# Kernel tuning notes

Hardware: AMD Instinct MI355X
Metric: run time of the kernel (lower is better)

Reference implementation:

```python
import jax, jax.numpy as jnp
import numpy as np

B, C, H, NH = 4, 512, 768, 12        # docs, seq len, hidden, attn heads
NE, MM = 20, 23                      # entities/doc, max mentions/entity
NP_ = NE * (NE - 1)                  # 380 head-tail pairs per doc
QS, POS, EMB, BLK, NB = 128, 128, 768, 64, 12
NCLS = 97
NEG = -10000.0

def _lin(k, i, o):
    return jax.random.normal(k, (i, o), jnp.float32) / np.sqrt(i)

def setup_inputs():
    key = jax.random.key(0)
    ks = jax.random.split(key, 24)
    seq = jax.random.normal(ks[0], (B, C, H), jnp.float32)
    att = jax.random.uniform(ks[1], (B, NH, C, C), jnp.float32)
    midx = jax.random.randint(ks[2], (B, NE, MM), 0, C)
    cnt = jax.random.randint(ks[3], (B, NE), 1, MM + 1)
    mmask = (jnp.arange(MM)[None, None, :] < cnt[:, :, None]).astype(jnp.float32)
    hh, tt = jnp.meshgrid(jnp.arange(NE), jnp.arange(NE), indexing='ij')
    off = ~jnp.eye(NE, dtype=bool)
    hts = jnp.stack([hh[off], tt[off]], -1)
    hts = jnp.broadcast_to(hts[None], (B, NP_, 2))
    vis = (jax.random.uniform(ks[4], (B, NP_, NP_)) > 0.3).astype(jnp.float32)
    inp = dict(sequence_output=seq, attention=att, mention_idx=midx,
               mention_mask=mmask, hts=hts, visible_mask=vis)
    wspec = [('Wcq', H, QS), ('Weq', H, QS), ('Whe', 2 * H, EMB), ('Wte', 2 * H, EMB),
             ('Wbl', EMB * BLK, EMB), ('Wpp', EMB + 2 * POS, EMB),
             ('Wgq', EMB, EMB), ('Wgk', EMB, EMB), ('Wgv', EMB, EMB),
             ('Wp1', 3 * EMB, EMB), ('Wp2', EMB, NCLS)]
    for j, (nm, i, o) in enumerate(wspec):
        inp[nm] = _lin(ks[5 + j], i, o)
        inp['b' + nm[1:]] = jnp.zeros((o,), jnp.float32)
    for nm in ('bgq', 'bgk', 'bgv'):
        inp.pop(nm)
    inp['pos_emb'] = jax.random.normal(ks[20], (42, POS), jnp.float32) * 0.02
    return inp

def reference(sequence_output, attention, mention_idx, mention_mask, hts, visible_mask,
              Wcq, bcq, Weq, beq, Whe, bhe, Wte, bte, Wbl, bbl, Wpp, bpp,
              Wgq, Wgk, Wgv, Wp1, bp1, Wp2, bp2, pos_emb):
    b3 = jnp.arange(B)[:, None, None]
    # per-entity mention gather (padded mentions zeroed, as in the torch loop)
    ent_emb = sequence_output[b3, mention_idx] * mention_mask[..., None]        # [B,NE,MM,H]
    att_t = jnp.transpose(attention, (0, 2, 1, 3))                              # [B,C,NH,C]
    ent_att = att_t[b3, mention_idx] * mention_mask[..., None, None]            # [B,NE,MM,NH,C]
    cnt = mention_mask.sum(-1)[..., None, None]
    ent_att = ent_att.sum(2) / cnt                                              # mean over valid mentions [B,NE,NH,C]

    bi = jnp.arange(B)[:, None]
    hi, ti = hts[..., 0], hts[..., 1]
    hs_m, ts_m = ent_emb[bi, hi], ent_emb[bi, ti]                               # [B,P,MM,H]
    hmask, tmask = mention_mask[bi, hi], mention_mask[bi, ti]                   # [B,P,MM]
    ht_att = (ent_att[bi, hi] * ent_att[bi, ti]).mean(2)                        # mean over heads [B,P,C]
    ht_att = ht_att / (ht_att.sum(-1, keepdims=True) + 1e-5)
    rs = jnp.einsum('bld,bpl->bpd', sequence_output, ht_att)                    # context [B,P,H]

    htq = rs @ Wcq + bcq                                                        # [B,P,QS]
    scale = 1.0 / np.sqrt(EMB)                                                  # original divides by sqrt(emb_size)
    G1 = jnp.einsum('bpq,bpmq->bpm', htq, hs_m @ Weq + beq) * scale
    G2 = jnp.einsum('bpq,bpmq->bpm', htq, ts_m @ Weq + beq) * scale
    G1 = jnp.where(hmask > 0, G1, NEG)
    G2 = jnp.where(tmask > 0, G2, NEG)
    hs = jnp.einsum('bpm,bpmh->bph', jax.nn.softmax(G1, -1), hs_m)
    ts = jnp.einsum('bpm,bpmh->bph', jax.nn.softmax(G2, -1), ts_m)

    hs = jnp.tanh(jnp.concatenate([hs, rs], -1) @ Whe + bhe)                    # [B,P,EMB]
    ts = jnp.tanh(jnp.concatenate([ts, rs], -1) @ Wte + bte)
    bh = hs.reshape(B, NP_, NB, BLK)
    bt = ts.reshape(B, NP_, NB, BLK)
    pair = (bh[..., :, None] * bt[..., None, :]).reshape(B, NP_, EMB * BLK)     # grouped bilinear feature
    pair = pair @ Wbl + bbl                                                     # [B,P,EMB]
    hs_core, ts_core = pos_emb[hi], pos_emb[ti]                                 # [B,P,POS]
    pair = jnp.tanh(jnp.concatenate([hs_core, pair, ts_core], -1) @ Wpp + bpp)

    # pair graph: one masked self-attention layer over pairs with residual
    q, k, v = pair @ Wgq, pair @ Wgk, pair @ Wgv
    sc = jnp.einsum('bpd,bqd->bpq', q, k) / np.sqrt(EMB)
    sc = jnp.where(visible_mask > 0, sc, NEG)
    pair = pair + jnp.einsum('bpq,bqd->bpd', jax.nn.softmax(sc, -1), v)

    feat = jnp.concatenate([hs, ts, pair], -1)                                  # [B,P,3*EMB]
    logits = jnp.tanh(feat @ Wp1 + bp1) @ Wp2 + bp2                             # dropout is identity at eval
    return logits.reshape(B * NP_, NCLS)
```

## Files before the change

kernel.cpp:

```cpp
#include <hip/hip_runtime.h>
#include <hip/hip_bf16.h>

#define Bn   4
#define Cn   512
#define Hn   768
#define NHn  12
#define NEn  20
#define MMn  23
#define Pn   380
#define Mr   1520
#define QSn  128
#define NEGV (-10000.0f)
#define SCL  0.036084391824351615f

typedef unsigned int uint32;
typedef __attribute__((ext_vector_type(8))) short short8;
typedef __attribute__((ext_vector_type(4))) float float4v;
typedef __attribute__((ext_vector_type(2))) _Float16 half2v;
typedef __attribute__((ext_vector_type(2))) __fp16 fp16x2;
typedef __attribute__((ext_vector_type(8))) _Float16 half8;

__device__ __forceinline__ unsigned short f2h(float f){
    return __builtin_bit_cast(unsigned short, (_Float16)f);
}
__device__ __forceinline__ uint32 pkrtz(float a, float b){
    fp16x2 h = __builtin_amdgcn_cvt_pkrtz(a, b);
    return __builtin_bit_cast(uint32, h);
}

static const size_t o_HS = 0;
static const size_t o_TS = 1167360;
static const size_t o_PB = 2334720;
static const size_t Xo   = 3502080;
static const size_t oEA = Xo;
static const size_t oEE = Xo+491520;
static const size_t oEK = Xo+1904640;
static const size_t oHA = Xo+2140160;
static const size_t oHQ = Xo+2918400;
static const size_t oSH = Xo+3112960;
static const size_t oST = Xo+4280320;
static const size_t oRS = Xo+5447680;
static const size_t oSEQT = Xo+6615040;
static const size_t oWCQ = Xo;
static const size_t oWEQ = Xo+49152;
static const size_t oWHE = Xo;
static const size_t oWTE = Xo+589824;
static const size_t oWBL = Xo;
static const size_t oFP = Xo;
static const size_t oPT = Xo+1556480;
static const size_t oQ  = Xo+2723840;
static const size_t oKT = Xo+3891200;
static const size_t oV  = Xo+5058560;
static const size_t oP2 = Xo+6225920;
static const size_t oT1 = Xo+7393280;
static const size_t oWPP = Xo+8560640;
static const size_t oWGQ = Xo+8953856;
static const size_t oWGK = Xo+9248768;
static const size_t oWGV = Xo+9543680;
static const size_t oWP1 = Xo+9838592;
static const size_t oWP2 = Xo+10723328;


__global__ __launch_bounds__(256) void k_ent_att(const float* __restrict__ att,
    const int* __restrict__ midx, const float* __restrict__ mmask, float* __restrict__ ea)
{
    int x = blockIdx.x;
    int nh = x % NHn; int e = (x / NHn) % NEn; int b = x / (NHn * NEn);
    __shared__ int   sidx[MMn];
    __shared__ float smsk[MMn];
    int t = threadIdx.x;
    if (t < MMn) { sidx[t] = midx[(b*NEn+e)*MMn + t]; smsk[t] = mmask[(b*NEn+e)*MMn + t]; }
    __syncthreads();
    float cnt = 0.f;
    for (int m = 0; m < MMn; m++) cnt += smsk[m];
    for (int c = t; c < Cn; c += 256) {
        float acc = 0.f;
        for (int m = 0; m < MMn; m++)
            acc += smsk[m] * att[((size_t)(b*NHn+nh)*Cn + sidx[m])*Cn + c];
        ea[(size_t)x*Cn + c] = acc / cnt;
    }
}

__global__ __launch_bounds__(256) void k_ent_emb(const float* __restrict__ seq,
    const int* __restrict__ midx, const float* __restrict__ mmask, float* __restrict__ ee)
{
    int x = blockIdx.x;
    int b = x / (NEn*MMn);
    int idx = midx[x]; float msk = mmask[x];
    int t = threadIdx.x;
    for (int h = t; h < Hn; h += 256)
        ee[(size_t)x*Hn + h] = msk * seq[((size_t)b*Cn + idx)*Hn + h];
}

__global__ __launch_bounds__(256) void k_htatt(const float* __restrict__ ea,
    const int* __restrict__ hts, float* __restrict__ hta)
{
    int row = blockIdx.x; int b = row / Pn;
    int he = hts[row*2], te = hts[row*2+1];
    __shared__ float sc[Cn];
    __shared__ float red[256];
    int t = threadIdx.x;
    const float* eah = ea + (size_t)(b*NEn+he)*NHn*Cn;
    const float* eat = ea + (size_t)(b*NEn+te)*NHn*Cn;
    for (int c = t; c < Cn; c += 256) {
        float a = 0.f;
        for (int nh = 0; nh < NHn; nh++) a += eah[nh*Cn+c]*eat[nh*Cn+c];
        sc[c] = a * (1.0f/NHn);
    }
    __syncthreads();
    float ps = sc[t] + sc[t+256];
    red[t] = ps; __syncthreads();
    for (int s = 128; s > 0; s >>= 1) { if (t < s) red[t] += red[t+s]; __syncthreads(); }
    float inv = 1.0f/(red[0] + 1e-5f);
    for (int c = t; c < Cn; c += 256) hta[(size_t)row*Cn + c] = sc[c]*inv;
}

__global__ __launch_bounds__(256) void k_select(const float* __restrict__ htq,
    const float* __restrict__ ekey, const float* __restrict__ ee,
    const float* __restrict__ mmask, const int* __restrict__ hts,
    float* __restrict__ selh, float* __restrict__ selt)
{
    int row = blockIdx.x; int side = blockIdx.y;
    int b = row / Pn;
    int e = hts[row*2 + side];
    __shared__ float qv[QSn];
    __shared__ float gsc[MMn];
    __shared__ float ew[MMn];
    int t = threadIdx.x;
    if (t < QSn) qv[t] = htq[(size_t)row*QSn + t];
    __syncthreads();
    if (t < MMn) {
        const float* kr = ekey + ((size_t)(b*NEn+e)*MMn + t)*QSn;
        float g = 0.f;
        for (int qq = 0; qq < QSn; qq++) g += qv[qq]*kr[qq];
        g *= SCL;
        float msk = mmask[(b*NEn+e)*MMn + t];
        gsc[t] = (msk > 0.f) ? g : NEGV;
    }
    __syncthreads();
    float mx = -1e30f;
    for (int m = 0; m < MMn; m++) mx = fmaxf(mx, gsc[m]);
    if (t < MMn) ew[t] = expf(gsc[t] - mx);
    __syncthreads();
    float s = 0.f;
    for (int m = 0; m < MMn; m++) s += ew[m];
    float invs = 1.0f/s;
    float* dst = side ? selt : selh;
    const float* eb = ee + (size_t)(b*NEn+e)*MMn*Hn;
    for (int h = t; h < Hn; h += 256) {
        float o = 0.f;
        for (int m = 0; m < MMn; m++) o += ew[m]*eb[(size_t)m*Hn + h];
        dst[(size_t)row*Hn + h] = o*invs;
    }
}

struct WD { const float* src; unsigned short* dst; int K; int N; int Npad; int t0; };
struct WT8 { WD d[8]; int nd; };

__global__ __launch_bounds__(256) void k_wtr(WT8 tab)
{
    int b = blockIdx.x;
    int i = 0;
    while (i+1 < tab.nd && b >= tab.d[i+1].t0) i++;
    WD d = tab.d[i];
    int tile = b - d.t0;
    int ktiles = d.K >> 6;
    int kt = tile % ktiles, nt = tile / ktiles;
    int k0 = kt*64, n0 = nt*64;
    __shared__ __align__(16) unsigned short tl[64][72];
    int t = threadIdx.x;
    int nl = t & 63, rq = t >> 6;
    #pragma unroll
    for (int r = 0; r < 16; r++) {
        int kl = r*4 + rq;
        float v = (n0+nl < d.N) ? d.src[(size_t)(k0+kl)*d.N + n0 + nl] : 0.f;
        tl[nl][kl] = f2h(v);
    }
    __syncthreads();
    int nn2 = t >> 2, kk0 = (t & 3) * 16;
    uint4 a = *(const uint4*)&tl[nn2][kk0];
    uint4 bq = *(const uint4*)&tl[nn2][kk0+8];
    uint4* dst = (uint4*)&d.dst[(size_t)(n0+nn2)*d.K + k0 + kk0];
    dst[0] = a; dst[1] = bq;
}

template<int MODE, int TM>
__global__ __launch_bounds__(256,4) void k_gmfma(
    const float* __restrict__ A0, const float* __restrict__ A1, const float* __restrict__ A2,
    int KA, int KB, int KC,
    const unsigned short* __restrict__ Wt,
    const float* __restrict__ bias, float* __restrict__ out,
    float* __restrict__ out2, float* __restrict__ out3,
    int Mtot, int N, int kchunk,
    long aStride, long wStride, long oStride)
{
    __shared__ __align__(16) unsigned short sa[64][72];
    __shared__ __align__(16) unsigned short sw[64][72];
    int t = threadIdx.x;
    int K = KA + KB + KC;
    int row0 = blockIdx.x * 64;
    int n0 = blockIdx.y * 64;
    int bz = blockIdx.z;
    const float* Ab = A0; const unsigned short* W = Wt; float* O = out;
    if (MODE & 32) { Ab += (size_t)bz*aStride; W += (size_t)bz*wStride; O += (size_t)bz*oStride; }
    int k0 = 0, k1 = K;
    if (MODE & 1) { k0 = bz*kchunk; k1 = k0 + kchunk; }
    int lane = t & 63, w = t >> 6, ln = lane & 15, q = lane >> 4;
    int sr = t >> 2;
    int sk = (t & 3) * 16;
    int rA = row0 + sr; if (rA > Mtot-1) rA = Mtot-1;

    float4v acc[4];
    #pragma unroll
    for (int mt = 0; mt < 4; mt++) acc[mt] = (float4v)0.f;

    for (int kk = k0; kk < k1; kk += 64) {
        const float* src; int kloc, Kl, seg;
        if (kk < KA)            { src = Ab; kloc = kk;          Kl = KA; seg = 0; }
        else if (kk < KA + KB)  { src = A1; kloc = kk - KA;     Kl = KB; seg = 1; }
        else                    { src = A2; kloc = kk - KA - KB; Kl = KC; seg = 2; }
        const float* ap = &src[(size_t)rA*Kl + kloc + sk];
        float4 v0 = ((const float4*)ap)[0];
        float4 v1 = ((const float4*)ap)[1];
        float4 v2 = ((const float4*)ap)[2];
        float4 v3 = ((const float4*)ap)[3];
        if (TM && ((TM >> seg) & 1)) {
            v0.x = tanhf(v0.x); v0.y = tanhf(v0.y); v0.z = tanhf(v0.z); v0.w = tanhf(v0.w);
            v1.x = tanhf(v1.x); v1.y = tanhf(v1.y); v1.z = tanhf(v1.z); v1.w = tanhf(v1.w);
            v2.x = tanhf(v2.x); v2.y = tanhf(v2.y); v2.z = tanhf(v2.z); v2.w = tanhf(v2.w);
            v3.x = tanhf(v3.x); v3.y = tanhf(v3.y); v3.z = tanhf(v3.z); v3.w = tanhf(v3.w);
        }
        const uint4* gw = (const uint4*)&W[(size_t)(n0+sr)*K + kk + sk];
        uint4 w0 = gw[0], w1 = gw[1];
        uint4 pa, pb;
        pa.x = pkrtz(v0.x, v0.y); pa.y = pkrtz(v0.z, v0.w);
        pa.z = pkrtz(v1.x, v1.y); pa.w = pkrtz(v1.z, v1.w);
        pb.x = pkrtz(v2.x, v2.y); pb.y = pkrtz(v2.z, v2.w);
        pb.z = pkrtz(v3.x, v3.y); pb.w = pkrtz(v3.z, v3.w);
        *(uint4*)&sa[sr][sk]   = pa;
        *(uint4*)&sa[sr][sk+8] = pb;
        *(uint4*)&sw[sr][sk]   = w0;
        *(uint4*)&sw[sr][sk+8] = w1;
        __syncthreads();
        half8 b0 = *(const half8*)&sw[w*16+ln][q*8];
        half8 b1 = *(const half8*)&sw[w*16+ln][32 + q*8];
        #pragma unroll
        for (int mt = 0; mt < 4; mt++) {
            half8 a0 = *(const half8*)&sa[mt*16+ln][q*8];
            half8 a1 = *(const half8*)&sa[mt*16+ln][32 + q*8];
            acc[mt] = __builtin_amdgcn_mfma_f32_16x16x32_f16(a0, b0, acc[mt], 0, 0, 0);
            acc[mt] = __builtin_amdgcn_mfma_f32_16x16x32_f16(a1, b1, acc[mt], 0, 0, 0);
        }
        __syncthreads();
    }
    int nn = n0 + w*16 + ln;
    if (MODE & 16) {
        int sg = nn / Hn; int nl = nn - sg*Hn;
        #pragma unroll
        for (int mt = 0; mt < 4; mt++) {
            #pragma unroll
            for (int r = 0; r < 4; r++) {
                int row = row0 + mt*16 + q*4 + r;
                if (row >= Mtot) continue;
                float val = acc[mt][r];
                if (sg == 0)      out [(size_t)row*Hn + nl] = val;
                else if (sg == 2) out3[(size_t)row*Hn + nl] = val;
                else {
                    int bb = row / Pn, pp = row % Pn;
                    out2[((size_t)bb*Hn + nl)*Pn + pp] = val;
                }
            }
        }
        return;
    }
    if (nn >= N) return;
    float bv = (MODE & 4) ? bias[nn] : 0.f;
    #pragma unroll
    for (int mt = 0; mt < 4; mt++) {
        #pragma unroll
        for (int r = 0; r < 4; r++) {
            int row = row0 + mt*16 + q*4 + r;
            if (row >= Mtot) continue;
            float val = acc[mt][r];
            if (MODE & 1) atomicAdd(&O[(size_t)row*N + nn], val);
            else          O[(size_t)row*N + nn] = val + bv;
        }
    }
}

__global__ __launch_bounds__(256) void k_binit(const float* __restrict__ bias,
    float* __restrict__ o, int N)
{
    int idx = blockIdx.x*256 + threadIdx.x;
    o[idx] = bias[idx % N];
}

__global__ __launch_bounds__(256) void k_binit3(const float* __restrict__ b0,
    const float* __restrict__ b1, const float* __restrict__ b2, float* __restrict__ o)
{
    int idx = blockIdx.x*256 + threadIdx.x;
    int r = idx / (Mr*Hn);
    const float* bb = (r == 0) ? b0 : ((r == 1) ? b1 : b2);
    o[idx] = bb[idx % Hn];
}

__global__ __launch_bounds__(256,4) void k_blmfma(const float* __restrict__ hs,
    const float* __restrict__ ts, const unsigned short* __restrict__ Wt,
    float* __restrict__ pb)
{
    __shared__ __align__(16) unsigned short hsl[64][72];
    __shared__ __align__(16) unsigned short tsl[64][72];
    __shared__ __align__(16) unsigned short ap[64][136];
    int t = threadIdx.x;
    int p0 = blockIdx.x * 64;
    int d0 = blockIdx.y * 128;
    int g  = blockIdx.z;
    int lane = t & 63, w = t >> 6, ln = lane & 15, q = lane >> 4;
    float4v acc[4][2];
    #pragma unroll
    for (int e = 0; e < 4; e++)
        #pragma unroll
        for (int f = 0; f < 2; f++) acc[e][f] = (float4v)0.f;
    const unsigned short* WtW = Wt + (size_t)(d0 + w*32)*49152;

    for (int nn = 0; nn < 2; nn++) {
        int n = 2*g + nn;
        {
            int p = t & 63; int c0 = (t >> 6) * 16;
            int pr = p0 + p; if (pr > Mr-1) pr = Mr-1;
            const float* hp = hs + (size_t)pr*Hn + n*64 + c0;
            const float* tp = ts + (size_t)pr*Hn + n*64 + c0;
            #pragma unroll
            for (int c = 0; c < 16; c++) {
                hsl[p][c0+c] = f2h(tanhf(hp[c]));
                tsl[p][c0+c] = f2h(tanhf(tp[c]));
            }
        }
        for (int i0 = 0; i0 < 64; i0 += 2) {
            __syncthreads();
            {
                int p = t & 63, sg = t >> 6;
                int ii = sg >> 1, j0 = (sg & 1) * 32;
                unsigned short hu = hsl[p][i0+ii];
                uint32 hrep = ((uint32)hu) | (((uint32)hu) << 16);
                half2v hv2 = __builtin_bit_cast(half2v, hrep);
                const uint4* tsrc = (const uint4*)&tsl[p][j0];
                uint4* dstp = (uint4*)&ap[p][ii*64 + j0];
                #pragma unroll
                for (int u = 0; u < 4; u++) {
                    uint4 tv = tsrc[u]; uint4 o;
                    o.x = __builtin_bit_cast(uint32, __builtin_bit_cast(half2v, tv.x) * hv2);
                    o.y = __builtin_bit_cast(uint32, __builtin_bit_cast(half2v, tv.y) * hv2);
                    o.z = __builtin_bit_cast(uint32, __builtin_bit_cast(half2v, tv.z) * hv2);
                    o.w = __builtin_bit_cast(uint32, __builtin_bit_cast(half2v, tv.w) * hv2);
                    dstp[u] = o;
                }
            }
            __syncthreads();
            size_t kbase = (size_t)n*4096 + (size_t)i0*64;
            #pragma unroll
            for (int c = 0; c < 4; c++) {
                half8 a[2], b[4];
                #pragma unroll
                for (int f = 0; f < 2; f++)
                    a[f] = *(const half8*)&WtW[(size_t)(f*16 + ln)*49152 + kbase + c*32 + q*8];
                #pragma unroll
                for (int e = 0; e < 4; e++)
                    b[e] = *(const half8*)&ap[e*16 + ln][c*32 + q*8];
                #pragma unroll
                for (int e = 0; e < 4; e++)
                    #pragma unroll
                    for (int f = 0; f < 2; f++)
                        acc[e][f] = __builtin_amdgcn_mfma_f32_16x16x32_f16(a[f], b[e], acc[e][f], 0, 0, 0);
            }
        }
        __syncthreads();
    }
    #pragma unroll
    for (int e = 0; e < 4; e++) {
        int p = p0 + e*16 + ln;
        if (p >= Mr) continue;
        #pragma unroll
        for (int f = 0; f < 2; f++) {
            int dbase = d0 + w*32 + f*16 + q*4;
            #pragma unroll
            for (int r = 0; r < 4; r++)
                atomicAdd(&pb[(size_t)p*Hn + dbase + r], acc[e][f][r]);
        }
    }
}


__global__ __launch_bounds__(256) void k_featpp(const float* __restrict__ pairbl,
    const float* __restrict__ pos, const int* __restrict__ hts, float* __restrict__ fpp)
{
    int row = blockIdx.x; int t = threadIdx.x;
    int he = hts[row*2], te = hts[row*2+1];
    float* dst = fpp + (size_t)row*1024;
    if (t < 128) { dst[t] = pos[he*128 + t]; dst[896 + t] = pos[te*128 + t]; }
    for (int h = t; h < Hn; h += 256) dst[128 + h] = pairbl[(size_t)row*Hn + h];
}

__global__ __launch_bounds__(256) void k_graph(const float* __restrict__ q,
    const float* __restrict__ kT, const float* __restrict__ v, const float* __restrict__ vis,
    const float* __restrict__ pairT, float* __restrict__ pair2)
{
    int row = blockIdx.x; int b = row / Pn; int p = row % Pn;
    __shared__ float qs[Hn];
    __shared__ float sc[Pn];
    __shared__ float red[256];
    int t = threadIdx.x;
    for (int h = t; h < Hn; h += 256) qs[h] = q[(size_t)row*Hn + h];
    __syncthreads();
    for (int qq = t; qq < Pn; qq += 256) {
        const float* kcol = kT + (size_t)b*Hn*Pn + qq;
        float a = 0.f;
        for (int h = 0; h < Hn; h++) a += qs[h]*kcol[(size_t)h*Pn];
        a *= SCL;
        float ms = vis[((size_t)b*Pn + p)*Pn + qq];
        sc[qq] = (ms > 0.f) ? a : NEGV;
    }
    __syncthreads();
    float mx = -1e30f;
    for (int qq = t; qq < Pn; qq += 256) mx = fmaxf(mx, sc[qq]);
    red[t] = mx; __syncthreads();
    for (int s = 128; s > 0; s >>= 1) { if (t < s) red[t] = fmaxf(red[t], red[t+s]); __syncthreads(); }
    mx = red[0];
    __syncthreads();
    float ps = 0.f;
    for (int qq = t; qq < Pn; qq += 256) { float e2 = expf(sc[qq]-mx); sc[qq] = e2; ps += e2; }
    red[t] = ps; __syncthreads();
    for (int s = 128; s > 0; s >>= 1) { if (t < s) red[t] += red[t+s]; __syncthreads(); }
    float invs = 1.0f/red[0];
    __syncthreads();
    float a0 = 0.f, a1 = 0.f, a2 = 0.f;
    for (int qq = 0; qq < Pn; qq++) {
        float sv = sc[qq];
        const float* vr = v + ((size_t)b*Pn+qq)*Hn + t;
        a0 += sv*vr[0]; a1 += sv*vr[256]; a2 += sv*vr[512];
    }
    const float* pt = pairT + (size_t)row*Hn + t;
    float* o = pair2 + (size_t)row*Hn + t;
    o[0]   = tanhf(pt[0])   + a0*invs;
    o[256] = tanhf(pt[256]) + a1*invs;
    o[512] = tanhf(pt[512]) + a2*invs;
}

__global__ __launch_bounds__(256) void k_fillu(unsigned int* p, unsigned int v, int n){
    int i = blockIdx.x*256 + threadIdx.x;
    if (i < n) p[i] = v;
}

extern "C" void kernel_launch(void* const* d_in, const int* in_sizes, int n_in,
                              void* d_out, int out_size, void* d_ws, size_t ws_size,
                              hipStream_t stream)
{
    const float* seq  = (const float*)d_in[0];
    const float* att  = (const float*)d_in[1];
    const int*   midx = (const int*)d_in[2];
    const float* mmask= (const float*)d_in[3];
    const int*   hts  = (const int*)d_in[4];
    const float* vis  = (const float*)d_in[5];
    const float* Wcq = (const float*)d_in[6];  const float* bcq = (const float*)d_in[7];
    const float* Weq = (const float*)d_in[8];  const float* beq = (const float*)d_in[9];
    const float* Whe = (const float*)d_in[10]; const float* bhe = (const float*)d_in[11];
    const float* Wte = (const float*)d_in[12]; const float* bte = (const float*)d_in[13];
    const float* Wbl = (const float*)d_in[14]; const float* bbl = (const float*)d_in[15];
    const float* Wpp = (const float*)d_in[16]; const float* bpp = (const float*)d_in[17];
    const float* Wgq = (const float*)d_in[18];
    const float* Wgk = (const float*)d_in[19];
    const float* Wgv = (const float*)d_in[20];
    const float* Wp1 = (const float*)d_in[21]; const float* bp1 = (const float*)d_in[22];
    const float* Wp2 = (const float*)d_in[23]; const float* bp2 = (const float*)d_in[24];
    const float* pos = (const float*)d_in[25];
    float* ws = (float*)d_ws;
    float* out = (float*)d_out;
    const float* nul = nullptr;
    float* nulw = nullptr;

    if (ws_size < 89505792ULL) {
        int n = out_size/2;
        k_fillu<<<(n+255)/256, 256, 0, stream>>>((unsigned int*)d_out, 0x476A476Au, n);
        return;
    }

    unsigned short* WCQt = (unsigned short*)(ws + oWCQ);
    unsigned short* WEQt = (unsigned short*)(ws + oWEQ);
    unsigned short* SEQt = (unsigned short*)(ws + oSEQT);
    unsigned short* WHEt = (unsigned short*)(ws + oWHE);
    unsigned short* WTEt = (unsigned short*)(ws + oWTE);
    unsigned short* WBLt = (unsigned short*)(ws + oWBL);
    unsigned short* WPPt = (unsigned short*)(ws + oWPP);
    unsigned short* WGQt = (unsigned short*)(ws + oWGQ);
    unsigned short* WP1t = (unsigned short*)(ws + oWP1);
    unsigned short* WP2t = (unsigned short*)(ws + oWP2);

    k_ent_att<<<Bn*NEn*NHn, 256, 0, stream>>>(att, midx, mmask, ws + oEA);
    k_ent_emb<<<Bn*NEn*MMn, 256, 0, stream>>>(seq, midx, mmask, ws + oEE);
    k_htatt<<<Mr, 256, 0, stream>>>(ws + oEA, hts, ws + oHA);

    {
        WT8 tb{}; tb.nd = 6;
        tb.d[0] = { Wcq, WCQt, 768, 128, 128, 0 };
        tb.d[1] = { Weq, WEQt, 768, 128, 128, 24 };
        for (int b = 0; b < 4; b++)
            tb.d[2+b] = { seq + (size_t)b*Cn*Hn, SEQt + (size_t)b*Hn*Cn, Cn, Hn, Hn, 48 + b*96 };
        k_wtr<<<432, 256, 0, stream>>>(tb);
    }
    k_gmfma<32,0><<<dim3(6,12,4), 256, 0, stream>>>(ws + oHA, nul, nul, Cn, 0, 0,
        SEQt, nul, ws + oRS, nulw, nulw, Pn, Hn, 0,
        (long)Pn*Cn, (long)Hn*Cn, (long)Pn*Hn);
    k_gmfma<4,0><<<dim3(24,2,1), 256, 0, stream>>>(ws + oRS, nul, nul, Hn, 0, 0,
        WCQt, bcq, ws + oHQ, nulw, nulw, Mr, QSn, 0, 0, 0, 0);
    k_gmfma<4,0><<<dim3(29,2,1), 256, 0, stream>>>(ws + oEE, nul, nul, Hn, 0, 0,
        WEQt, beq, ws + oEK, nulw, nulw, Bn*NEn*MMn, QSn, 0, 0, 0, 0);
    k_select<<<dim3(Mr,2), 256, 0, stream>>>(ws + oHQ, ws + oEK, ws + oEE,
        mmask, hts, ws + oSH, ws + oST);

    {
        WT8 tb{}; tb.nd = 2;
        tb.d[0] = { Whe, WHEt, 1536, 768, 768, 0 };
        tb.d[1] = { Wte, WTEt, 1536, 768, 768, 288 };
        k_wtr<<<576, 256, 0, stream>>>(tb);
    }
    k_binit3<<<(3*Mr*Hn)/256, 256, 0, stream>>>(bhe, bte, bbl, ws + o_HS);
    k_gmfma<1,0><<<dim3(24,12,3), 256, 0, stream>>>(ws + oSH, ws + oRS, nul, Hn, Hn, 0,
        WHEt, nul, ws + o_HS, nulw, nulw, Mr, Hn, 512, 0, 0, 0);
    k_gmfma<1,0><<<dim3(24,12,3), 256, 0, stream>>>(ws + oST, ws + oRS, nul, Hn, Hn, 0,
        WTEt, nul, ws + o_TS, nulw, nulw, Mr, Hn, 512, 0, 0, 0);

    {
        WT8 tb{}; tb.nd = 1;
        tb.d[0] = { Wbl, WBLt, 49152, 768, 768, 0 };
        k_wtr<<<9216, 256, 0, stream>>>(tb);
    }
    k_blmfma<<<dim3(24,6,6), 256, 0, stream>>>(ws + o_HS, ws + o_TS, WBLt, ws + o_PB);

    k_featpp<<<Mr, 256, 0, stream>>>(ws + o_PB, pos, hts, ws + oFP);

    {
        WT8 tb{}; tb.nd = 6;
        tb.d[0] = { Wpp, WPPt, 1024, 768, 768, 0 };
        tb.d[1] = { Wgq, WGQt, 768, 768, 768, 192 };
        tb.d[2] = { Wgk, (unsigned short*)(ws + oWGK), 768, 768, 768, 336 };
        tb.d[3] = { Wgv, (unsigned short*)(ws + oWGV), 768, 768, 768, 480 };
        tb.d[4] = { Wp1, WP1t, 2304, 768, 768, 624 };
        tb.d[5] = { Wp2, WP2t, 768, 97, 128, 1056 };
        k_wtr<<<1080, 256, 0, stream>>>(tb);
    }
    k_binit<<<(Mr*Hn)/256, 256, 0, stream>>>(bpp, ws + oPT, Hn);
    k_gmfma<1,0><<<dim3(24,12,2), 256, 0, stream>>>(ws + oFP, nul, nul, 1024, 0, 0,
        WPPt, nul, ws + oPT, nulw, nulw, Mr, Hn, 512, 0, 0, 0);
    k_gmfma<16,1><<<dim3(24,36,1), 256, 0, stream>>>(ws + oPT, nul, nul, Hn, 0, 0,
        WGQt, nul, ws + oQ, ws + oKT, ws + oV, Mr, 3*Hn, 0, 0, 0, 0);
    k_graph<<<Mr, 256, 0, stream>>>(ws + oQ, ws + oKT, ws + oV, vis, ws + oPT, ws + oP2);
    k_binit<<<(Mr*Hn)/256, 256, 0, stream>>>(bp1, ws + oT1, Hn);
    k_gmfma<1,3><<<dim3(24,12,3), 256, 0, stream>>>(ws + o_HS, ws + o_TS, ws + oP2,
        Hn, Hn, Hn, WP1t, nul, ws + oT1, nulw, nulw, Mr, Hn, 768, 0, 0, 0);
    k_gmfma<4,1><<<dim3(24,2,1), 256, 0, stream>>>(ws + oT1, nul, nul, Hn, 0, 0,
        WP2t, bp2, out, nulw, nulw, Mr, 97, 0, 0, 0, 0);
}
```

Before: 1.074 ms.

## Build bilinear outer-product operands in registers instead of staging through shared memory

The grouped bilinear MFMA kernel stops writing the hs⊗ts outer product into a shared-memory tile on every i0 step, which needed two barriers per step. Each thread now keeps its ts fragments in registers and multiplies them by a splatted hs scalar right before each MFMA. It also vectorizes the tanh/fp16 conversion loads and remaps block IDs into a swizzled order so blocks that share weight rows run close together for better L2 reuse. In exchange it uses more registers and spends extra packed multiplies per MFMA.

```diff
diff --git a/kernel.cpp b/kernel.cpp
--- a/kernel.cpp
+++ b/kernel.cpp
@@ -14,7 +14,6 @@
 #define SCL  0.036084391824351615f
 
 typedef unsigned int uint32;
-typedef __attribute__((ext_vector_type(8))) short short8;
 typedef __attribute__((ext_vector_type(4))) float float4v;
 typedef __attribute__((ext_vector_type(2))) _Float16 half2v;
 typedef __attribute__((ext_vector_type(2))) __fp16 fp16x2;
@@ -26,6 +25,14 @@
 __device__ __forceinline__ uint32 pkrtz(float a, float b){
     fp16x2 h = __builtin_amdgcn_cvt_pkrtz(a, b);
     return __builtin_bit_cast(uint32, h);
+}
+__device__ __forceinline__ half8 mulsplat(half8 a, uint32 hd){
+    half2v s = __builtin_bit_cast(half2v, hd);
+    union { half8 h; half2v c[4]; } u, v;
+    u.h = a;
+    #pragma unroll
+    for (int i = 0; i < 4; i++) v.c[i] = u.c[i] * s;
+    return v.h;
 }
 
 static const size_t o_HS = 0;
@@ -308,73 +315,83 @@
     const float* __restrict__ ts, const unsigned short* __restrict__ Wt,
     float* __restrict__ pb)
 {
-    __shared__ __align__(16) unsigned short hsl[64][72];
-    __shared__ __align__(16) unsigned short tsl[64][72];
-    __shared__ __align__(16) unsigned short ap[64][136];
-    int t = threadIdx.x;
-    int p0 = blockIdx.x * 64;
-    int d0 = blockIdx.y * 128;
-    int g  = blockIdx.z;
+    __shared__ __align__(16) unsigned short hsl[2][64][72];
+    __shared__ __align__(16) unsigned short tsl[2][64][72];
+    int t = threadIdx.x;
+    int bid = blockIdx.x + 24*(blockIdx.y + 6*blockIdx.z);
+    int sb = (bid & 7)*108 + (bid >> 3);
+    int p_t = sb % 24; int r2 = sb / 24;
+    int p0 = p_t * 64;
+    int d0 = (r2 % 6) * 128;
+    int g  = r2 / 6;
     int lane = t & 63, w = t >> 6, ln = lane & 15, q = lane >> 4;
     float4v acc[4][2];
     #pragma unroll
     for (int e = 0; e < 4; e++)
         #pragma unroll
         for (int f = 0; f < 2; f++) acc[e][f] = (float4v)0.f;
-    const unsigned short* WtW = Wt + (size_t)(d0 + w*32)*49152;
+    const unsigned short* WtW = Wt + (size_t)(d0 + w*32)*49152 + q*8;
+    const unsigned short* wb0 = WtW + (size_t)ln*49152;
+    const unsigned short* wb1 = WtW + (size_t)(16+ln)*49152;
 
     for (int nn = 0; nn < 2; nn++) {
         int n = 2*g + nn;
+        __syncthreads();
         {
             int p = t & 63; int c0 = (t >> 6) * 16;
             int pr = p0 + p; if (pr > Mr-1) pr = Mr-1;
             const float* hp = hs + (size_t)pr*Hn + n*64 + c0;
             const float* tp = ts + (size_t)pr*Hn + n*64 + c0;
+            float4 h0 = ((const float4*)hp)[0], h1 = ((const float4*)hp)[1];
+            float4 h2 = ((const float4*)hp)[2], h3 = ((const float4*)hp)[3];
+            float4 t0 = ((const float4*)tp)[0], t1 = ((const float4*)tp)[1];
+            float4 t2 = ((const float4*)tp)[2], t3 = ((const float4*)tp)[3];
+            uint4 ha, hb, ta, tb;
+            ha.x = pkrtz(tanhf(h0.x), tanhf(h0.y)); ha.y = pkrtz(tanhf(h0.z), tanhf(h0.w));
+            ha.z = pkrtz(tanhf(h1.x), tanhf(h1.y)); ha.w = pkrtz(tanhf(h1.z), tanhf(h1.w));
+            hb.x = pkrtz(tanhf(h2.x), tanhf(h2.y)); hb.y = pkrtz(tanhf(h2.z), tanhf(h2.w));
+            hb.z = pkrtz(tanhf(h3.x), tanhf(h3.y)); hb.w = pkrtz(tanhf(h3.z), tanhf(h3.w));
+            ta.x = pkrtz(tanhf(t0.x), tanhf(t0.y)); ta.y = pkrtz(tanhf(t0.z), tanhf(t0.w));
+            ta.z = pkrtz(tanhf(t1.x), tanhf(t1.y)); ta.w = pkrtz(tanhf(t1.z), tanhf(t1.w));
+            tb.x = pkrtz(tanhf(t2.x), tanhf(t2.y)); tb.y = pkrtz(tanhf(t2.z), tanhf(t2.w));
+            tb.z = pkrtz(tanhf(t3.x), tanhf(t3.y)); tb.w = pkrtz(tanhf(t3.z), tanhf(t3.w));
+            *(uint4*)&hsl[nn][p][c0]   = ha; *(uint4*)&hsl[nn][p][c0+8] = hb;
+            *(uint4*)&tsl[nn][p][c0]   = ta; *(uint4*)&tsl[nn][p][c0+8] = tb;
+        }
+        __syncthreads();
+        half8 tsr[4][2];
+        #pragma unroll
+        for (int e = 0; e < 4; e++) {
+            tsr[e][0] = *(const half8*)&tsl[nn][e*16+ln][q*8];
+            tsr[e][1] = *(const half8*)&tsl[nn][e*16+ln][32 + q*8];
+        }
+        const unsigned short* w0p = wb0 + (size_t)n*4096;
+        const unsigned short* w1p = wb1 + (size_t)n*4096;
+        for (int i0 = 0; i0 < 64; i0 += 2) {
+            uint4 aw0[4], aw1[4];
             #pragma unroll
-            for (int c = 0; c < 16; c++) {
-                hsl[p][c0+c] = f2h(tanhf(hp[c]));
-                tsl[p][c0+c] = f2h(tanhf(tp[c]));
+            for (int c = 0; c < 4; c++) {
+                aw0[c] = *(const uint4*)(w0p + i0*64 + c*32);
+                aw1[c] = *(const uint4*)(w1p + i0*64 + c*32);
             }
-        }
-        for (int i0 = 0; i0 < 64; i0 += 2) {
-            __syncthreads();
-            {
-                int p = t & 63, sg = t >> 6;
-                int ii = sg >> 1, j0 = (sg & 1) * 32;
-                unsigned short hu = hsl[p][i0+ii];
-                uint32 hrep = ((uint32)hu) | (((uint32)hu) << 16);
-                half2v hv2 = __builtin_bit_cast(half2v, hrep);
-                const uint4* tsrc = (const uint4*)&tsl[p][j0];
-                uint4* dstp = (uint4*)&ap[p][ii*64 + j0];
+            uint32 hw[4];
+            #pragma unroll
+            for (int e = 0; e < 4; e++)
+                hw[e] = *(const uint32*)&hsl[nn][e*16+ln][i0];
+            #pragma unroll
+            for (int c = 0; c < 4; c++) {
                 #pragma unroll
-                for (int u = 0; u < 4; u++) {
-                    uint4 tv = tsrc[u]; uint4 o;
-                    o.x = __builtin_bit_cast(uint32, __builtin_bit_cast(half2v, tv.x) * hv2);
-                    o.y = __builtin_bit_cast(uint32, __builtin_bit_cast(half2v, tv.y) * hv2);
-                    o.z = __builtin_bit_cast(uint32, __builtin_bit_cast(half2v, tv.z) * hv2);
-                    o.w = __builtin_bit_cast(uint32, __builtin_bit_cast(half2v, tv.w) * hv2);
-                    dstp[u] = o;
+                for (int e = 0; e < 4; e++) {
+                    uint32 hu = (c & 2) ? (hw[e] >> 16) : (hw[e] & 0xFFFFu);
+                    uint32 hd = hu | (hu << 16);
+                    half8 bfr = mulsplat(tsr[e][c & 1], hd);
+                    acc[e][0] = __builtin_amdgcn_mfma_f32_16x16x32_f16(
+                        __builtin_bit_cast(half8, aw0[c]), bfr, acc[e][0], 0, 0, 0);
+                    acc[e][1] = __builtin_amdgcn_mfma_f32_16x16x32_f16(
+                        __builtin_bit_cast(half8, aw1[c]), bfr, acc[e][1], 0, 0, 0);
                 }
             }
-            __syncthreads();
-            size_t kbase = (size_t)n*4096 + (size_t)i0*64;
-            #pragma unroll
-            for (int c = 0; c < 4; c++) {
-                half8 a[2], b[4];
-                #pragma unroll
-                for (int f = 0; f < 2; f++)
-                    a[f] = *(const half8*)&WtW[(size_t)(f*16 + ln)*49152 + kbase + c*32 + q*8];
-                #pragma unroll
-                for (int e = 0; e < 4; e++)
-                    b[e] = *(const half8*)&ap[e*16 + ln][c*32 + q*8];
-                #pragma unroll
-                for (int e = 0; e < 4; e++)
-                    #pragma unroll
-                    for (int f = 0; f < 2; f++)
-                        acc[e][f] = __builtin_amdgcn_mfma_f32_16x16x32_f16(a[f], b[e], acc[e][f], 0, 0, 0);
-            }
-        }
-        __syncthreads();
+        }
     }
     #pragma unroll
     for (int e = 0; e < 4; e++) {
```

Result: faster. 1.031 ms (-4.0%).
